# Optimization experiments

Measured on AMD Instinct MI355X. Metric: run time of the kernel, lower is better.

Reference implementation:

```python
import jax, jax.numpy as jnp
import numpy as np

B, M, H, R = 4096, 4, 1024, 10
MID, D3 = 512, 3 * H  # gate MLP mid = max(32, H//2)
AUDIO = 1
OTHERS = (0, 2, 3)


def _ln(x, w, b):
    m = jnp.mean(x, axis=-1, keepdims=True)
    v = jnp.mean((x - m) ** 2, axis=-1, keepdims=True)
    return (x - m) * jax.lax.rsqrt(v + 1e-5) * w + b


def _gate(t, s, lw, lb, w1, b1, w2, b2):
    feat = jnp.concatenate([t, s, jnp.abs(t - s)], axis=-1)  # [..., 3H]
    h = jax.nn.gelu(_ln(feat, lw, lb) @ w1.T + b1, approximate=False)
    return jax.nn.sigmoid(h @ w2.T + b2)  # [..., 1]


def setup_inputs() -> dict:
    key = jax.random.key(0)
    ks = jax.random.split(key, 16)
    xn = lambda k, shp, fan: jax.random.normal(k, shp, jnp.float32) * (1.0 / np.sqrt(fan))
    inp = {
        'tokens': jax.random.normal(ks[0], (B, M, H), jnp.float32),
        'token_mask': jax.random.randint(ks[1], (B, M), 0, 2) > 0,
        # gate_other: LayerNorm(3H) -> Linear(3H,MID) -> GELU -> Linear(MID,1)
        'ln_go_w': jnp.ones((D3,), jnp.float32), 'ln_go_b': jnp.zeros((D3,), jnp.float32),
        'go_w1': xn(ks[2], (MID, D3), D3), 'go_b1': jnp.zeros((MID,), jnp.float32),
        'go_w2': xn(ks[3], (1, MID), MID), 'go_b2': jnp.zeros((1,), jnp.float32),
        # gate_audio
        'ln_ga_w': jnp.ones((D3,), jnp.float32), 'ln_ga_b': jnp.zeros((D3,), jnp.float32),
        'ga_w1': xn(ks[4], (MID, D3), D3), 'ga_b1': jnp.zeros((MID,), jnp.float32),
        'ga_w2': xn(ks[5], (1, MID), MID), 'ga_b2': jnp.zeros((1,), jnp.float32),
        'a2o_w': xn(ks[6], (H, H), H), 'o2a_w': xn(ks[7], (H, H), H),
        'ln_o_w': jnp.ones((H,), jnp.float32), 'ln_o_b': jnp.zeros((H,), jnp.float32),
        'ln_a_w': jnp.ones((H,), jnp.float32), 'ln_a_b': jnp.zeros((H,), jnp.float32),
        # LMF
        'factors': jax.random.normal(ks[8], (M, R, H + 1, H), jnp.float32) * np.sqrt(2.0 / (H + 1 + H)),
        'rank_w': jax.random.normal(ks[9], (R,), jnp.float32) * 0.02,
        'lmf_bias': jnp.zeros((H,), jnp.float32),
        'out_ln1_w': jnp.ones((H,), jnp.float32), 'out_ln1_b': jnp.zeros((H,), jnp.float32),
        'out_w': xn(ks[10], (H, H), H), 'out_b': jnp.zeros((H,), jnp.float32),
        'out_ln2_w': jnp.ones((H,), jnp.float32), 'out_ln2_b': jnp.zeros((H,), jnp.float32),
    }
    return inp


def reference(tokens, token_mask, ln_go_w, ln_go_b, go_w1, go_b1, go_w2, go_b2,
              ln_ga_w, ln_ga_b, ga_w1, ga_b1, ga_w2, ga_b2, a2o_w, o2a_w,
              ln_o_w, ln_o_b, ln_a_w, ln_a_b, factors, rank_w, lmf_bias,
              out_ln1_w, out_ln1_b, out_w, out_b, out_ln2_w, out_ln2_b):
    mask_f = token_mask.astype(tokens.dtype)  # [B, M]
    oidx = jnp.asarray(OTHERS)

    # ---- AudioGuidedResidualMixer (eval mode) ----
    audio = tokens[:, AUDIO]                          # [B, H]
    audio_valid = token_mask[:, AUDIO]                # [B]
    others = tokens[:, oidx] * mask_f[:, oidx, None]  # [B, 3, H] (masked targets)
    src = jnp.broadcast_to(audio[:, None, :], others.shape)
    g = _gate(others, src, ln_go_w, ln_go_b, go_w1, go_b1, go_w2, go_b2)  # [B,3,1]
    a2o = audio @ a2o_w.T                                                  # [B, H]
    upd = _ln(others + g * a2o[:, None, :], ln_o_w, ln_o_b)
    pair_valid = token_mask[:, oidx] & audio_valid[:, None]                # [B, 3]
    others_new = jnp.where(pair_valid[..., None], upd, others) * mask_f[:, oidx, None]

    w_o = mask_f[:, oidx, None]
    denom = jnp.clip(w_o.sum(axis=1), 1.0, None)
    others_mean = (others_new * w_o).sum(axis=1) / denom                   # [B, H]
    aum = audio_valid & token_mask[:, oidx].any(axis=1)                    # [B]
    g_a = _gate(audio, others_mean, ln_ga_w, ln_ga_b, ga_w1, ga_b1, ga_w2, ga_b2)
    o2a = others_mean @ o2a_w.T
    mixed_audio = jnp.where(aum[:, None],
                            _ln(audio + g_a * o2a, ln_a_w, ln_a_b),
                            audio * mask_f[:, AUDIO, None])
    mixed = jnp.stack([others_new[:, 0], mixed_audio, others_new[:, 1], others_new[:, 2]],
                      axis=1) * mask_f[..., None]                          # [B, M, H]

    # ---- LowRankMultiplicativeFusion ----
    one = jnp.ones((mixed.shape[0], M, 1), mixed.dtype)
    x_aug = jnp.concatenate([one, mixed], axis=-1)                         # [B, M, H+1]
    z = jnp.einsum('bmd,mrdh->bmrh', x_aug, factors)                       # [B, M, R, H]
    z = jnp.where(token_mask[:, :, None, None], z, jnp.ones((), z.dtype))
    rank_tensor = jnp.prod(z, axis=1)                                      # [B, R, H]
    fused = jnp.einsum('brh,r->bh', rank_tensor, rank_w) + lmf_bias
    h = _ln(fused, out_ln1_w, out_ln1_b)
    h = jax.nn.gelu(h @ out_w.T + out_b, approximate=False)
    return _ln(h, out_ln2_w, out_ln2_b)                                    # [B, H]
```

## Files before the change

kernel.cpp:

```cpp
#include <hip/hip_runtime.h>
#include <math.h>

#define BB 4096
#define HH 1024
#define RR 10
#define MIDD 512
#define D3 3072

typedef __bf16 bf16x8 __attribute__((ext_vector_type(8)));
typedef __bf16 bf16x4 __attribute__((ext_vector_type(4)));
typedef float f32x4 __attribute__((ext_vector_type(4)));

__device__ __forceinline__ float waveSum(float v){
#pragma unroll
  for(int o=32;o>0;o>>=1) v += __shfl_down(v,o,64);
  return v;
}
__device__ __forceinline__ float blockSum256(float v, float* sc){
  v = waveSum(v);
  __syncthreads();
  if((threadIdx.x & 63)==0) sc[threadIdx.x>>6] = v;
  __syncthreads();
  return sc[0]+sc[1]+sc[2]+sc[3];
}
__device__ __forceinline__ float gelu_f(float x){
  return 0.5f*x*(1.0f+erff(x*0.70710678118654752f));
}
__device__ __forceinline__ void gl_lds16(const void* g, void* lds){
  __builtin_amdgcn_global_load_lds((const __attribute__((address_space(1))) unsigned int*)g,
                                   (__attribute__((address_space(3))) unsigned int*)lds,
                                   16, 0, 0);
}

__global__ void convw_k(const float* __restrict__ s0, __bf16* __restrict__ d0, int n0,
                        const float* __restrict__ s1, __bf16* __restrict__ d1, int n1,
                        const float* __restrict__ s2, __bf16* __restrict__ d2, int n2,
                        const float* __restrict__ s3, __bf16* __restrict__ d3, int n3,
                        const float* __restrict__ s4, __bf16* __restrict__ d4, int n4){
  long i = ((long)blockIdx.x*256 + threadIdx.x)*4;
  const float* s; __bf16* d;
  if(i<n0){ s=s0; d=d0; }
  else { i-=n0; if(i<n1){ s=s1; d=d1; }
  else { i-=n1; if(i<n2){ s=s2; d=d2; }
  else { i-=n2; if(i<n3){ s=s3; d=d3; }
  else { i-=n3; if(i>=n4) return; s=s4; d=d4; } } } }
  float4 v=*(const float4*)(s+i);
  bf16x4 o; o[0]=(__bf16)v.x; o[1]=(__bf16)v.y; o[2]=(__bf16)v.z; o[3]=(__bf16)v.w;
  *(bf16x4*)(d+i)=o;
}

__global__ void feat_go_k(const float* __restrict__ tokens, const int* __restrict__ mask,
                          const float* __restrict__ lnw, const float* __restrict__ lnb,
                          __bf16* __restrict__ featGo, __bf16* __restrict__ audioB,
                          float* __restrict__ gpre){
  int row=blockIdx.x; int b=row/3; int j=row-b*3; int oj=(j==0)?0:(j+1);
  if(threadIdx.x==0) gpre[row]=0.f;
  const float* to=tokens+((size_t)b*4+oj)*HH;
  const float* ta=tokens+((size_t)b*4+1)*HH;
  float mo = mask[b*4+oj]?1.f:0.f;
  int tid=threadIdx.x;
  __shared__ float sc[4];
  float ov[4], av[4], dv[4]; float s=0.f,s2=0.f;
#pragma unroll
  for(int p=0;p<4;p++){
    int h=tid+p*256;
    float o=to[h]*mo, a=ta[h], d=fabsf(o-a);
    ov[p]=o; av[p]=a; dv[p]=d;
    s+=o+a+d; s2+=o*o+a*a+d*d;
  }
  s=blockSum256(s,sc); s2=blockSum256(s2,sc);
  float mean=s/(float)D3, rstd=rsqrtf(s2/(float)D3-mean*mean+1e-5f);
  __bf16* fr = featGo + (size_t)row*D3;
#pragma unroll
  for(int p=0;p<4;p++){
    int h=tid+p*256;
    fr[h]       =(__bf16)((ov[p]-mean)*rstd*lnw[h]+lnb[h]);
    fr[1024+h]  =(__bf16)((av[p]-mean)*rstd*lnw[1024+h]+lnb[1024+h]);
    fr[2048+h]  =(__bf16)((dv[p]-mean)*rstd*lnw[2048+h]+lnb[2048+h]);
    if(j==0) audioB[(size_t)b*HH+h]=(__bf16)av[p];
  }
}

template<int ACT>
__launch_bounds__(256, 4)
__global__ void gemm_nt_mfma(const __bf16* __restrict__ A, int lda,
                             const __bf16* __restrict__ Bm, int ldb,
                             const float* __restrict__ bias,
                             float* __restrict__ C, int ldc, int K,
                             const float* __restrict__ w2,
                             float* __restrict__ gpre){
  __shared__ __align__(16) __bf16 As[3*2048];
  __shared__ __align__(16) __bf16 Bs[3*4096];
  const int tid=threadIdx.x, l=tid&63, w=tid>>6;
  const int wr=w>>1, wc=w&1;
  const int quad=l>>4, lr16=l&15;

  const int nbx = gridDim.x;
  const int flat = blockIdx.x + nbx*blockIdx.y;
  const int chunk = (nbx*gridDim.y)>>3;
  const int nid = (flat&7)*chunk + (flat>>3);
  const int bx = nid % nbx, by = nid / nbx;
  const int row0=by*64, col0=bx*128;

  const int srow=l>>2, sq=(l&3)^((l>>3)&3);
  const int nsteps = K>>5;

  const __bf16* pa  = A  + (size_t)(row0 + w*16       + srow)*lda + sq*8;
  const __bf16* pb0 = Bm + (size_t)(col0 + w*16       + srow)*ldb + sq*8;
  const __bf16* pb1 = Bm + (size_t)(col0 + (w+4)*16   + srow)*ldb + sq*8;
  __bf16* da  = As + ((size_t)w*64     + l)*8;
  __bf16* db0 = Bs + ((size_t)w*64     + l)*8;
  __bf16* db1 = Bs + ((size_t)(w+4)*64 + l)*8;

  auto stage=[&](int s,int bi){
    int k0 = s*32;
    gl_lds16(pa  + k0, da  + bi*2048);
    gl_lds16(pb0 + k0, db0 + bi*4096);
    gl_lds16(pb1 + k0, db1 + bi*4096);
  };

  f32x4 acc[2][4];
  f32x4 zerov={0.f,0.f,0.f,0.f};
#pragma unroll
  for(int i=0;i<2;i++)
#pragma unroll
    for(int j=0;j<4;j++) acc[i][j]=zerov;

  stage(0,0);
  stage(1,1);
  asm volatile("s_waitcnt vmcnt(3)" ::: "memory");
  __builtin_amdgcn_s_barrier();

  int cur=0;
  for(int step=0; step<nsteps; ++step){
    const __bf16* Ab = As + cur*2048;
    const __bf16* Bb = Bs + cur*4096;
    bf16x8 af[2], bg[4];
#pragma unroll
    for(int fi=0;fi<2;fi++){
      int R = wr*32 + fi*16 + lr16;
      af[fi]=*(const bf16x8*)(Ab + R*32 + ((quad^(R>>1))&3)*8);
    }
#pragma unroll
    for(int fj=0;fj<4;fj++){
      int N = wc*64 + fj*16 + lr16;
      bg[fj]=*(const bf16x8*)(Bb + N*32 + ((quad^(N>>1))&3)*8);
    }
    if(step+2<nsteps){
      int bi = cur + 2; if(bi>=3) bi-=3;
      stage(step+2, bi);
    }
    __builtin_amdgcn_s_setprio(1);
#pragma unroll
    for(int fi=0;fi<2;fi++)
#pragma unroll
      for(int fj=0;fj<4;fj++)
        acc[fi][fj]=__builtin_amdgcn_mfma_f32_16x16x32_bf16(af[fi],bg[fj],acc[fi][fj],0,0,0);
    __builtin_amdgcn_s_setprio(0);
    asm volatile("s_waitcnt lgkmcnt(0)" ::: "memory");
    if(step < nsteps-2) asm volatile("s_waitcnt vmcnt(3)" ::: "memory");
    else                asm volatile("s_waitcnt vmcnt(0)" ::: "memory");
    __builtin_amdgcn_s_barrier();
    cur = (cur+1==3)?0:cur+1;
  }

  if(ACT==2){
    float b1v[4], w2v[4];
#pragma unroll
    for(int fj=0;fj<4;fj++){
      int col=col0+wc*64+fj*16+lr16;
      b1v[fj]=bias[col]; w2v[fj]=w2[col];
    }
#pragma unroll
    for(int fi=0;fi<2;fi++){
#pragma unroll
      for(int reg=0;reg<4;reg++){
        float part=0.f;
#pragma unroll
        for(int fj=0;fj<4;fj++) part += gelu_f(acc[fi][fj][reg]+b1v[fj])*w2v[fj];
        part += __shfl_xor(part,1,64);
        part += __shfl_xor(part,2,64);
        part += __shfl_xor(part,4,64);
        part += __shfl_xor(part,8,64);
        if((l&15)==0) atomicAdd(&gpre[row0+wr*32+fi*16+quad*4+reg], part);
      }
    }
    return;
  }

  float bv[4];
#pragma unroll
  for(int fj=0;fj<4;fj++) bv[fj] = (ACT==1)? bias[col0+wc*64+fj*16+lr16] : 0.f;
#pragma unroll
  for(int fi=0;fi<2;fi++){
#pragma unroll
    for(int reg=0;reg<4;reg++){
      int row=row0+wr*32+fi*16+quad*4+reg;
#pragma unroll
      for(int fj=0;fj<4;fj++){
        int col=col0+wc*64+fj*16+lr16;
        float v=acc[fi][fj][reg];
        if(ACT==1) v=gelu_f(v+bv[fj]);
        C[(size_t)row*ldc+col]=v;
      }
    }
  }
}

__global__ void others_k(const float* __restrict__ tokens, const int* __restrict__ mask,
                         const float* __restrict__ gpre, const float* __restrict__ go_b2,
                         const float* __restrict__ a2o,
                         const float* __restrict__ lnw, const float* __restrict__ lnb,
                         const float* __restrict__ galnw, const float* __restrict__ galnb,
                         __bf16* __restrict__ mixedB, __bf16* __restrict__ omeanB,
                         __bf16* __restrict__ featGa, float* __restrict__ gapre){
  int b=blockIdx.x, tid=threadIdx.x;
  __shared__ float sc[4];
  if(tid==0) gapre[b]=0.f;
  float ma = mask[b*4+1]?1.f:0.f;
  float a2[4];
#pragma unroll
  for(int p=0;p<4;p++) a2[p]=a2o[(size_t)b*HH+tid+p*256];
  float sum[4]={0,0,0,0}; float cnt=0.f;
  for(int j=0;j<3;j++){
    int oj=(j==0)?0:(j+1);
    float mo=mask[b*4+oj]?1.f:0.f; cnt+=mo;
    float gv=1.f/(1.f+expf(-(gpre[b*3+j]+go_b2[0])));
    float t[4], ov[4]; float s=0.f,s2=0.f;
#pragma unroll
    for(int p=0;p<4;p++){
      int h=tid+p*256;
      float o=tokens[((size_t)b*4+oj)*HH+h]*mo;
      ov[p]=o; t[p]=o+gv*a2[p];
      s+=t[p]; s2+=t[p]*t[p];
    }
    s=blockSum256(s,sc); s2=blockSum256(s2,sc);
    float mean=s/1024.f, rstd=rsqrtf(s2/1024.f-mean*mean+1e-5f);
    float pv=mo*ma;
#pragma unroll
    for(int p=0;p<4;p++){
      int h=tid+p*256;
      float upd=(t[p]-mean)*rstd*lnw[h]+lnb[h];
      float on=((pv>0.5f)?upd:ov[p])*mo;
      mixedB[(size_t)b*4096 + (size_t)oj*HH + h]=(__bf16)on;
      sum[p]+=on*mo;
    }
  }
  float denom=fmaxf(cnt,1.f);
  float vm[4];
#pragma unroll
  for(int p=0;p<4;p++){
    vm[p]=sum[p]/denom;
    omeanB[(size_t)b*HH+tid+p*256]=(__bf16)vm[p];
  }
  const float* ta=tokens+((size_t)b*4+1)*HH;
  float tv[4], dv[4]; float s=0.f,s2=0.f;
#pragma unroll
  for(int p=0;p<4;p++){
    int h=tid+p*256;
    float a=ta[h], d=fabsf(a-vm[p]);
    tv[p]=a; dv[p]=d;
    s+=a+vm[p]+d; s2+=a*a+vm[p]*vm[p]+d*d;
  }
  s=blockSum256(s,sc); s2=blockSum256(s2,sc);
  float mean=s/(float)D3, rstd=rsqrtf(s2/(float)D3-mean*mean+1e-5f);
  __bf16* fr=featGa+(size_t)b*D3;
#pragma unroll
  for(int p=0;p<4;p++){
    int h=tid+p*256;
    fr[h]     =(__bf16)((tv[p]-mean)*rstd*galnw[h]+galnb[h]);
    fr[1024+h]=(__bf16)((vm[p]-mean)*rstd*galnw[1024+h]+galnb[1024+h]);
    fr[2048+h]=(__bf16)((dv[p]-mean)*rstd*galnw[2048+h]+galnb[2048+h]);
  }
}

__global__ void audio_k(const float* __restrict__ tokens, const int* __restrict__ mask,
                        const float* __restrict__ gapre, const float* __restrict__ ga_b2,
                        const float* __restrict__ o2a,
                        const float* __restrict__ lnw, const float* __restrict__ lnb,
                        __bf16* __restrict__ mixedB,
                        const float* __restrict__ lmf_bias, float* __restrict__ fused){
  int b=blockIdx.x, tid=threadIdx.x;
  __shared__ float sc[4];
  int ma_i=mask[b*4+1];
  int any = mask[b*4+0]|mask[b*4+2]|mask[b*4+3];
  bool aum = (ma_i!=0) && (any!=0);
  float ma = ma_i?1.f:0.f;
  float gv=1.f/(1.f+expf(-(gapre[b]+ga_b2[0])));
  const float* ta = tokens + ((size_t)b*4+1)*HH;
  float av[4], t[4]; float s=0.f,s2=0.f;
#pragma unroll
  for(int p=0;p<4;p++){
    int h=tid+p*256;
    av[p]=ta[h];
    t[p]=av[p]+gv*o2a[(size_t)b*HH+h];
    s+=t[p]; s2+=t[p]*t[p];
  }
  s=blockSum256(s,sc); s2=blockSum256(s2,sc);
  float mean=s/1024.f, rstd=rsqrtf(s2/1024.f-mean*mean+1e-5f);
#pragma unroll
  for(int p=0;p<4;p++){
    int h=tid+p*256;
    float u=(t[p]-mean)*rstd*lnw[h]+lnb[h];
    float outv = aum ? u : av[p]*ma;
    mixedB[(size_t)b*4096 + HH + h]=(__bf16)(outv*ma);
    fused[(size_t)b*HH + h]=lmf_bias[h];
  }
}

__global__ void transpose_factors_k(const float* __restrict__ factors,
                                    __bf16* __restrict__ factT){
  __shared__ float T[64][65];
  int mr = blockIdx.z;
  int d0 = blockIdx.y*64, h0 = blockIdx.x*64;
  int t = threadIdx.x;
  int rr = t>>4, cc = (t&15)*4;
  const float* src = factors + ((size_t)mr*1025 + 1 + d0)*1024 + h0;
#pragma unroll
  for(int q=0;q<4;q++){
    float4 v = *(const float4*)(src + (size_t)(q*16+rr)*1024 + cc);
    T[q*16+rr][cc]=v.x; T[q*16+rr][cc+1]=v.y; T[q*16+rr][cc+2]=v.z; T[q*16+rr][cc+3]=v.w;
  }
  __syncthreads();
  __bf16* dst = factT + ((size_t)mr*1024 + h0)*1024 + d0;
#pragma unroll
  for(int q=0;q<4;q++){
    int hr = q*16 + rr;
    bf16x4 o;
    o[0]=(__bf16)T[cc][hr];   o[1]=(__bf16)T[cc+1][hr];
    o[2]=(__bf16)T[cc+2][hr]; o[3]=(__bf16)T[cc+3][hr];
    *(bf16x4*)(dst + (size_t)hr*1024 + cc) = o;
  }
}

__launch_bounds__(256, 2)
__global__ void gemm_lmf2(const __bf16* __restrict__ mixedB,
                          const __bf16* __restrict__ factT,
                          const float* __restrict__ factors,
                          const int* __restrict__ mask,
                          const float* __restrict__ rank_w,
                          float* __restrict__ fused){
  __shared__ __align__(16) __bf16 As[3*4096];
  __shared__ __align__(16) __bf16 Bs[3*4096];
  __shared__ float Mskf[4][128];
  __shared__ float F0s[20][128];
  __shared__ float Rws[5];
  const int tid = threadIdx.x;
  const int l = tid & 63, w = tid >> 6;
  const int wr = w >> 1, wc = w & 1;
  const int quad = l >> 4, lr16 = l & 15;

  const int flat = blockIdx.x + 8*(blockIdx.y + 32*blockIdx.z);
  const int nid  = (flat & 7)*64 + (flat >> 3);
  const int hh   = nid >> 6;
  const int rest = nid & 63;
  const int by   = rest >> 1;
  const int bz   = rest & 1;
  const int row0 = by * 128, col0 = hh * 128;
  const int z5   = bz * 5;

  const int srow = l >> 2;
  const int sq   = (l & 3) ^ ((l >> 3) & 3);

  for(int i = tid; i < 512; i += 256){
    int mm = i >> 7, rl = i & 127;
    Mskf[mm][rl] = mask[(row0 + rl)*4 + mm] ? 1.f : 0.f;
  }
  for(int i = tid; i < 2560; i += 256){
    int rm = i >> 7, cl = i & 127;
    int m = rm & 3, rg = z5 + (rm >> 2);
    F0s[rm][cl] = factors[(size_t)(m*RR + rg)*1025*1024 + col0 + cl];
  }
  if(tid < 5) Rws[tid] = rank_w[z5 + tid];

  const __bf16* pa0 = mixedB + (size_t)(row0 + w*16     + srow)*4096 + sq*8;
  const __bf16* pa1 = mixedB + (size_t)(row0 + (w+4)*16 + srow)*4096 + sq*8;
  const __bf16* pb0 = factT + ((size_t)(col0 + w*16     + srow))*1024 + sq*8;
  const __bf16* pb1 = factT + ((size_t)(col0 + (w+4)*16 + srow))*1024 + sq*8;
  __bf16* da0 = As + ((size_t)w*64     + l)*8;
  __bf16* da1 = As + ((size_t)(w+4)*64 + l)*8;
  __bf16* db0 = Bs + ((size_t)w*64     + l)*8;
  __bf16* db1 = Bs + ((size_t)(w+4)*64 + l)*8;

  auto stage = [&](int s, int bi){
    int rm = s >> 5, k0 = (s & 31)*32;
    int m = rm & 3, rg = z5 + (rm >> 2);
    size_t ao = (size_t)m*1024 + k0;
    size_t bo = (size_t)(m*RR + rg)*1048576 + k0;
    gl_lds16(pa0 + ao, da0 + bi*4096);
    gl_lds16(pa1 + ao, da1 + bi*4096);
    gl_lds16(pb0 + bo, db0 + bi*4096);
    gl_lds16(pb1 + bo, db1 + bi*4096);
  };

  f32x4 fsum[4][4];
  f32x4 prod[4][4];
  f32x4 acc[4][4];
  f32x4 zerov = {0.f,0.f,0.f,0.f};
#pragma unroll
  for(int i=0;i<4;i++)
#pragma unroll
    for(int j=0;j<4;j++) fsum[i][j] = zerov;

  stage(0, 0);
  stage(1, 1);
  asm volatile("s_waitcnt vmcnt(4)" ::: "memory");
  asm volatile("s_waitcnt lgkmcnt(0)" ::: "memory");
  __builtin_amdgcn_s_barrier();

  int cur = 0;
  for(int step = 0; step < 640; ++step){
    const __bf16* Ab = As + cur*4096;
    const __bf16* Bb = Bs + cur*4096;
    bf16x8 af[4], bg[4];
#pragma unroll
    for(int fi=0;fi<4;fi++){
      int R = wr*64 + fi*16 + lr16;
      af[fi] = *(const bf16x8*)(Ab + R*32 + ((quad ^ (R>>1)) & 3)*8);
    }
#pragma unroll
    for(int fj=0;fj<4;fj++){
      int N = wc*64 + fj*16 + lr16;
      bg[fj] = *(const bf16x8*)(Bb + N*32 + ((quad ^ (N>>1)) & 3)*8);
    }
    if(step + 2 < 640){
      int bi = cur + 2; if(bi >= 3) bi -= 3;
      stage(step + 2, bi);
    }
    if((step & 127) == 0){
      f32x4 onev = {1.f,1.f,1.f,1.f};
#pragma unroll
      for(int fi=0;fi<4;fi++)
#pragma unroll
        for(int fj=0;fj<4;fj++) prod[fi][fj] = onev;
    }
    if((step & 31) == 0){
      int rm = step >> 5;
#pragma unroll
      for(int fj=0;fj<4;fj++){
        float f0 = F0s[rm][wc*64 + fj*16 + lr16];
        f32x4 iv = {f0,f0,f0,f0};
#pragma unroll
        for(int fi=0;fi<4;fi++) acc[fi][fj] = iv;
      }
    }
    __builtin_amdgcn_s_setprio(1);
#pragma unroll
    for(int fi=0;fi<4;fi++)
#pragma unroll
      for(int fj=0;fj<4;fj++)
        acc[fi][fj] = __builtin_amdgcn_mfma_f32_16x16x32_bf16(af[fi], bg[fj], acc[fi][fj], 0,0,0);
    __builtin_amdgcn_s_setprio(0);
    if((step & 31) == 31){
      int mm = (step >> 5) & 3;
#pragma unroll
      for(int fi=0;fi<4;fi++)
#pragma unroll
        for(int reg=0;reg<4;reg++){
          float mk = Mskf[mm][wr*64 + fi*16 + quad*4 + reg];
#pragma unroll
          for(int fj=0;fj<4;fj++)
            prod[fi][fj][reg] *= (mk != 0.f) ? acc[fi][fj][reg] : 1.f;
        }
    }
    if((step & 127) == 127){
      float rw = Rws[step >> 7];
#pragma unroll
      for(int fi=0;fi<4;fi++)
#pragma unroll
        for(int fj=0;fj<4;fj++)
#pragma unroll
          for(int reg=0;reg<4;reg++)
            fsum[fi][fj][reg] += rw * prod[fi][fj][reg];
    }
    asm volatile("s_waitcnt lgkmcnt(0)" ::: "memory");
    if(step < 638) asm volatile("s_waitcnt vmcnt(4)" ::: "memory");
    else           asm volatile("s_waitcnt vmcnt(0)" ::: "memory");
    __builtin_amdgcn_s_barrier();
    cur = (cur + 1 == 3) ? 0 : cur + 1;
  }

#pragma unroll
  for(int fi=0;fi<4;fi++){
#pragma unroll
    for(int reg=0;reg<4;reg++){
      int row = row0 + wr*64 + fi*16 + quad*4 + reg;
#pragma unroll
      for(int fj=0;fj<4;fj++){
        int col = col0 + wc*64 + fj*16 + lr16;
        atomicAdd(&fused[(size_t)row*HH + col], fsum[fi][fj][reg]);
      }
    }
  }
}

__global__ void ln_row_k(const float* __restrict__ X, const float* __restrict__ w,
                         const float* __restrict__ bb, float* __restrict__ Y){
  int b=blockIdx.x, tid=threadIdx.x;
  __shared__ float sc[4];
  const float* x=X+(size_t)b*HH;
  float t[4]; float s=0.f,s2=0.f;
#pragma unroll
  for(int p=0;p<4;p++){ t[p]=x[tid+p*256]; s+=t[p]; s2+=t[p]*t[p]; }
  s=blockSum256(s,sc); s2=blockSum256(s2,sc);
  float mean=s/1024.f, rstd=rsqrtf(s2/1024.f-mean*mean+1e-5f);
#pragma unroll
  for(int p=0;p<4;p++){
    int h=tid+p*256;
    Y[(size_t)b*HH+h]=(t[p]-mean)*rstd*w[h]+bb[h];
  }
}
__global__ void ln_row_bf16_k(const float* __restrict__ X, const float* __restrict__ w,
                              const float* __restrict__ bb, __bf16* __restrict__ Y){
  int b=blockIdx.x, tid=threadIdx.x;
  __shared__ float sc[4];
  const float* x=X+(size_t)b*HH;
  float t[4]; float s=0.f,s2=0.f;
#pragma unroll
  for(int p=0;p<4;p++){ t[p]=x[tid+p*256]; s+=t[p]; s2+=t[p]*t[p]; }
  s=blockSum256(s,sc); s2=blockSum256(s2,sc);
  float mean=s/1024.f, rstd=rsqrtf(s2/1024.f-mean*mean+1e-5f);
#pragma unroll
  for(int p=0;p<4;p++){
    int h=tid+p*256;
    Y[(size_t)b*HH+h]=(__bf16)((t[p]-mean)*rstd*w[h]+bb[h]);
  }
}

extern "C" void kernel_launch(void* const* d_in, const int* in_sizes, int n_in,
                              void* d_out, int out_size, void* d_ws, size_t ws_size,
                              hipStream_t stream) {
  const float* tokens   =(const float*)d_in[0];
  const int*   mask     =(const int*)  d_in[1];
  const float* ln_go_w  =(const float*)d_in[2];
  const float* ln_go_b  =(const float*)d_in[3];
  const float* go_w1    =(const float*)d_in[4];
  const float* go_b1    =(const float*)d_in[5];
  const float* go_w2    =(const float*)d_in[6];
  const float* go_b2    =(const float*)d_in[7];
  const float* ln_ga_w  =(const float*)d_in[8];
  const float* ln_ga_b  =(const float*)d_in[9];
  const float* ga_w1    =(const float*)d_in[10];
  const float* ga_b1    =(const float*)d_in[11];
  const float* ga_w2    =(const float*)d_in[12];
  const float* ga_b2    =(const float*)d_in[13];
  const float* a2o_w    =(const float*)d_in[14];
  const float* o2a_w    =(const float*)d_in[15];
  const float* ln_o_w   =(const float*)d_in[16];
  const float* ln_o_b   =(const float*)d_in[17];
  const float* ln_a_w   =(const float*)d_in[18];
  const float* ln_a_b   =(const float*)d_in[19];
  const float* factors  =(const float*)d_in[20];
  const float* rank_w   =(const float*)d_in[21];
  const float* lmf_bias =(const float*)d_in[22];
  const float* out_ln1_w=(const float*)d_in[23];
  const float* out_ln1_b=(const float*)d_in[24];
  const float* out_w    =(const float*)d_in[25];
  const float* out_b    =(const float*)d_in[26];
  const float* out_ln2_w=(const float*)d_in[27];
  const float* out_ln2_b=(const float*)d_in[28];
  float* out=(float*)d_out;

  char* wsp=(char*)d_ws; size_t off=0;
  auto alloc=[&](size_t bytes)->void*{
    void* p=wsp+off; off=(off+bytes+255)&~(size_t)255; return p;
  };
  __bf16* factT   =(__bf16*)alloc((size_t)4*RR*HH*HH*2);
  __bf16* featGo  =(__bf16*)alloc((size_t)BB*3*D3*2);
  __bf16* featGa  =(__bf16*)alloc((size_t)BB*D3*2);
  float*  g_go_pre=(float*) alloc((size_t)BB*3*4);
  float*  ga_pre  =(float*) alloc((size_t)BB*4);
  float*  a2o     =(float*) alloc((size_t)BB*HH*4);
  __bf16* mixedB  =(__bf16*)alloc((size_t)BB*4*HH*2);
  __bf16* omeanB  =(__bf16*)alloc((size_t)BB*HH*2);
  __bf16* audioB  =(__bf16*)alloc((size_t)BB*HH*2);
  float*  o2a     =(float*) alloc((size_t)BB*HH*4);
  float*  fused   =(float*) alloc((size_t)BB*HH*4);
  __bf16* hbufB   =(__bf16*)alloc((size_t)BB*HH*2);
  __bf16* go_w1B  =(__bf16*)alloc((size_t)MIDD*D3*2);
  __bf16* ga_w1B  =(__bf16*)alloc((size_t)MIDD*D3*2);
  __bf16* a2o_wB  =(__bf16*)alloc((size_t)HH*HH*2);
  __bf16* o2a_wB  =(__bf16*)alloc((size_t)HH*HH*2);
  __bf16* out_wB  =(__bf16*)alloc((size_t)HH*HH*2);

  {
    int n0=MIDD*D3, n1=MIDD*D3, n2=HH*HH, n3=HH*HH, n4=HH*HH;
    int total4=(n0+n1+n2+n3+n4)/4;
    convw_k<<<(total4+255)/256,256,0,stream>>>(go_w1,go_w1B,n0, ga_w1,ga_w1B,n1,
                                               a2o_w,a2o_wB,n2, o2a_w,o2a_wB,n3,
                                               out_w,out_wB,n4);
  }
  transpose_factors_k<<<dim3(16,16,40),256,0,stream>>>(factors,factT);
  feat_go_k<<<BB*3,256,0,stream>>>(tokens,mask,ln_go_w,ln_go_b,featGo,audioB,g_go_pre);
  gemm_nt_mfma<0><<<dim3(8,64),256,0,stream>>>(audioB,HH,a2o_wB,HH,nullptr,a2o,HH,HH,nullptr,nullptr);
  gemm_nt_mfma<2><<<dim3(4,192),256,0,stream>>>(featGo,D3,go_w1B,D3,go_b1,nullptr,0,D3,go_w2,g_go_pre);
  others_k<<<BB,256,0,stream>>>(tokens,mask,g_go_pre,go_b2,a2o,ln_o_w,ln_o_b,
                                ln_ga_w,ln_ga_b,mixedB,omeanB,featGa,ga_pre);
  gemm_nt_mfma<2><<<dim3(4,64),256,0,stream>>>(featGa,D3,ga_w1B,D3,ga_b1,nullptr,0,D3,ga_w2,ga_pre);
  gemm_nt_mfma<0><<<dim3(8,64),256,0,stream>>>(omeanB,HH,o2a_wB,HH,nullptr,o2a,HH,HH,nullptr,nullptr);
  audio_k<<<BB,256,0,stream>>>(tokens,mask,ga_pre,ga_b2,o2a,ln_a_w,ln_a_b,mixedB,lmf_bias,fused);
  gemm_lmf2<<<dim3(8,32,2),256,0,stream>>>(mixedB,factT,factors,mask,rank_w,fused);
  ln_row_bf16_k<<<BB,256,0,stream>>>(fused,out_ln1_w,out_ln1_b,hbufB);
  gemm_nt_mfma<1><<<dim3(8,64),256,0,stream>>>(hbufB,HH,out_wB,HH,out_b,fused,HH,HH,nullptr,nullptr);
  ln_row_k<<<BB,256,0,stream>>>(fused,out_ln2_w,out_ln2_b,out);
}
```

Baseline: 1.021 ms.

## Merge prep kernels and pair independent GEMMs into combined launches

Weight conversion, factor transposition and gate-feature LayerNorm are folded into one prep kernel selected by block index. Independent GEMM pairs (a2o with gate_other hidden, gate_audio hidden with o2a) run in one launch through a runtime descriptor, so they fill the GPU together and pay fewer launch gaps. The LMF GEMM block-to-tile mapping is also reordered for locality. The GEMM activation mode becomes a runtime branch instead of a template parameter, which may cost registers or code quality.

```diff
diff --git a/kernel.cpp b/kernel.cpp
--- a/kernel.cpp
+++ b/kernel.cpp
@@ -32,82 +32,118 @@
                                    16, 0, 0);
 }
 
-__global__ void convw_k(const float* __restrict__ s0, __bf16* __restrict__ d0, int n0,
-                        const float* __restrict__ s1, __bf16* __restrict__ d1, int n1,
-                        const float* __restrict__ s2, __bf16* __restrict__ d2, int n2,
-                        const float* __restrict__ s3, __bf16* __restrict__ d3, int n3,
-                        const float* __restrict__ s4, __bf16* __restrict__ d4, int n4){
-  long i = ((long)blockIdx.x*256 + threadIdx.x)*4;
-  const float* s; __bf16* d;
-  if(i<n0){ s=s0; d=d0; }
-  else { i-=n0; if(i<n1){ s=s1; d=d1; }
-  else { i-=n1; if(i<n2){ s=s2; d=d2; }
-  else { i-=n2; if(i<n3){ s=s3; d=d3; }
-  else { i-=n3; if(i>=n4) return; s=s4; d=d4; } } } }
-  float4 v=*(const float4*)(s+i);
-  bf16x4 o; o[0]=(__bf16)v.x; o[1]=(__bf16)v.y; o[2]=(__bf16)v.z; o[3]=(__bf16)v.w;
-  *(bf16x4*)(d+i)=o;
-}
-
-__global__ void feat_go_k(const float* __restrict__ tokens, const int* __restrict__ mask,
-                          const float* __restrict__ lnw, const float* __restrict__ lnb,
-                          __bf16* __restrict__ featGo, __bf16* __restrict__ audioB,
-                          float* __restrict__ gpre){
-  int row=blockIdx.x; int b=row/3; int j=row-b*3; int oj=(j==0)?0:(j+1);
-  if(threadIdx.x==0) gpre[row]=0.f;
-  const float* to=tokens+((size_t)b*4+oj)*HH;
-  const float* ta=tokens+((size_t)b*4+1)*HH;
-  float mo = mask[b*4+oj]?1.f:0.f;
-  int tid=threadIdx.x;
-  __shared__ float sc[4];
-  float ov[4], av[4], dv[4]; float s=0.f,s2=0.f;
-#pragma unroll
-  for(int p=0;p<4;p++){
-    int h=tid+p*256;
-    float o=to[h]*mo, a=ta[h], d=fabsf(o-a);
-    ov[p]=o; av[p]=a; dv[p]=d;
-    s+=o+a+d; s2+=o*o+a*a+d*d;
-  }
-  s=blockSum256(s,sc); s2=blockSum256(s2,sc);
-  float mean=s/(float)D3, rstd=rsqrtf(s2/(float)D3-mean*mean+1e-5f);
-  __bf16* fr = featGo + (size_t)row*D3;
-#pragma unroll
-  for(int p=0;p<4;p++){
-    int h=tid+p*256;
-    fr[h]       =(__bf16)((ov[p]-mean)*rstd*lnw[h]+lnb[h]);
-    fr[1024+h]  =(__bf16)((av[p]-mean)*rstd*lnw[1024+h]+lnb[1024+h]);
-    fr[2048+h]  =(__bf16)((dv[p]-mean)*rstd*lnw[2048+h]+lnb[2048+h]);
-    if(j==0) audioB[(size_t)b*HH+h]=(__bf16)av[p];
-  }
-}
-
-template<int ACT>
+__global__ void prep_k(const float* __restrict__ go_w1, __bf16* __restrict__ go_w1B,
+                       const float* __restrict__ ga_w1, __bf16* __restrict__ ga_w1B,
+                       const float* __restrict__ a2o_w, __bf16* __restrict__ a2o_wB,
+                       const float* __restrict__ o2a_w, __bf16* __restrict__ o2a_wB,
+                       const float* __restrict__ out_w, __bf16* __restrict__ out_wB,
+                       const float* __restrict__ factors, __bf16* __restrict__ factT,
+                       const float* __restrict__ tokens, const int* __restrict__ mask,
+                       const float* __restrict__ lnw, const float* __restrict__ lnb,
+                       __bf16* __restrict__ featGo, __bf16* __restrict__ audioB,
+                       float* __restrict__ gpre){
+  __shared__ float T[64][65];
+  const int b = blockIdx.x;
+  const int tid = threadIdx.x;
+
+  if(b < 6144){
+    const int n0=MIDD*D3, n1=MIDD*D3, n2=HH*HH, n3=HH*HH, n4=HH*HH;
+    long i = ((long)b*256 + tid)*4;
+    const float* s; __bf16* d;
+    if(i<n0){ s=go_w1; d=go_w1B; }
+    else { i-=n0; if(i<n1){ s=ga_w1; d=ga_w1B; }
+    else { i-=n1; if(i<n2){ s=a2o_w; d=a2o_wB; }
+    else { i-=n2; if(i<n3){ s=o2a_w; d=o2a_wB; }
+    else { i-=n3; if(i>=n4) return; s=out_w; d=out_wB; } } } }
+    float4 v=*(const float4*)(s+i);
+    bf16x4 o; o[0]=(__bf16)v.x; o[1]=(__bf16)v.y; o[2]=(__bf16)v.z; o[3]=(__bf16)v.w;
+    *(bf16x4*)(d+i)=o;
+    return;
+  }
+  if(b < 16384){
+    int id = b - 6144;
+    int h0 = (id & 15)*64;
+    int d0 = ((id >> 4) & 15)*64;
+    int mr = id >> 8;
+    int rr = tid>>4, cc = (tid&15)*4;
+    const float* src = factors + ((size_t)mr*1025 + 1 + d0)*1024 + h0;
+#pragma unroll
+    for(int q=0;q<4;q++){
+      float4 v = *(const float4*)(src + (size_t)(q*16+rr)*1024 + cc);
+      T[q*16+rr][cc]=v.x; T[q*16+rr][cc+1]=v.y; T[q*16+rr][cc+2]=v.z; T[q*16+rr][cc+3]=v.w;
+    }
+    __syncthreads();
+    __bf16* dst = factT + ((size_t)mr*1024 + h0)*1024 + d0;
+#pragma unroll
+    for(int q=0;q<4;q++){
+      int hr = q*16 + rr;
+      bf16x4 o;
+      o[0]=(__bf16)T[cc][hr];   o[1]=(__bf16)T[cc+1][hr];
+      o[2]=(__bf16)T[cc+2][hr]; o[3]=(__bf16)T[cc+3][hr];
+      *(bf16x4*)(dst + (size_t)hr*1024 + cc) = o;
+    }
+    return;
+  }
+  {
+    int row = b - 16384;
+    int bb_ = row/3; int j = row - bb_*3; int oj = (j==0)?0:(j+1);
+    if(tid==0) gpre[row]=0.f;
+    const float* to=tokens+((size_t)bb_*4+oj)*HH;
+    const float* ta=tokens+((size_t)bb_*4+1)*HH;
+    float mo = mask[bb_*4+oj]?1.f:0.f;
+    float* sc = &T[0][0];
+    float ov[4], av[4], dv[4]; float s=0.f,s2=0.f;
+#pragma unroll
+    for(int p=0;p<4;p++){
+      int h=tid+p*256;
+      float o=to[h]*mo, a=ta[h], d=fabsf(o-a);
+      ov[p]=o; av[p]=a; dv[p]=d;
+      s+=o+a+d; s2+=o*o+a*a+d*d;
+    }
+    s=blockSum256(s,sc); s2=blockSum256(s2,sc);
+    float mean=s/(float)D3, rstd=rsqrtf(s2/(float)D3-mean*mean+1e-5f);
+    __bf16* fr = featGo + (size_t)row*D3;
+#pragma unroll
+    for(int p=0;p<4;p++){
+      int h=tid+p*256;
+      fr[h]       =(__bf16)((ov[p]-mean)*rstd*lnw[h]+lnb[h]);
+      fr[1024+h]  =(__bf16)((av[p]-mean)*rstd*lnw[1024+h]+lnb[1024+h]);
+      fr[2048+h]  =(__bf16)((dv[p]-mean)*rstd*lnw[2048+h]+lnb[2048+h]);
+      if(j==0) audioB[(size_t)bb_*HH+h]=(__bf16)av[p];
+    }
+  }
+}
+
+struct GD {
+  const __bf16* A; const __bf16* B;
+  const float* bias; float* C;
+  const float* w2; float* gpre;
+  int lda, ldb, ldc, K, nbx, nby, act;
+};
+
 __launch_bounds__(256, 4)
-__global__ void gemm_nt_mfma(const __bf16* __restrict__ A, int lda,
-                             const __bf16* __restrict__ Bm, int ldb,
-                             const float* __restrict__ bias,
-                             float* __restrict__ C, int ldc, int K,
-                             const float* __restrict__ w2,
-                             float* __restrict__ gpre){
+__global__ void gemm_dual_k(GD d0, GD d1, int n0){
   __shared__ __align__(16) __bf16 As[3*2048];
   __shared__ __align__(16) __bf16 Bs[3*4096];
   const int tid=threadIdx.x, l=tid&63, w=tid>>6;
   const int wr=w>>1, wc=w&1;
   const int quad=l>>4, lr16=l&15;
 
-  const int nbx = gridDim.x;
-  const int flat = blockIdx.x + nbx*blockIdx.y;
-  const int chunk = (nbx*gridDim.y)>>3;
-  const int nid = (flat&7)*chunk + (flat>>3);
-  const int bx = nid % nbx, by = nid / nbx;
+  GD d; int lb;
+  if((int)blockIdx.x < n0){ d = d0; lb = blockIdx.x; }
+  else                    { d = d1; lb = blockIdx.x - n0; }
+
+  const int chunk = (d.nbx*d.nby)>>3;
+  const int nid = (lb&7)*chunk + (lb>>3);
+  const int bx = nid % d.nbx, by = nid / d.nbx;
   const int row0=by*64, col0=bx*128;
 
   const int srow=l>>2, sq=(l&3)^((l>>3)&3);
-  const int nsteps = K>>5;
-
-  const __bf16* pa  = A  + (size_t)(row0 + w*16       + srow)*lda + sq*8;
-  const __bf16* pb0 = Bm + (size_t)(col0 + w*16       + srow)*ldb + sq*8;
-  const __bf16* pb1 = Bm + (size_t)(col0 + (w+4)*16   + srow)*ldb + sq*8;
+  const int nsteps = d.K>>5;
+
+  const __bf16* pa  = d.A + (size_t)(row0 + w*16       + srow)*d.lda + sq*8;
+  const __bf16* pb0 = d.B + (size_t)(col0 + w*16       + srow)*d.ldb + sq*8;
+  const __bf16* pb1 = d.B + (size_t)(col0 + (w+4)*16   + srow)*d.ldb + sq*8;
   __bf16* da  = As + ((size_t)w*64     + l)*8;
   __bf16* db0 = Bs + ((size_t)w*64     + l)*8;
   __bf16* db1 = Bs + ((size_t)(w+4)*64 + l)*8;
@@ -164,12 +200,12 @@
     cur = (cur+1==3)?0:cur+1;
   }
 
-  if(ACT==2){
+  if(d.act==2){
     float b1v[4], w2v[4];
 #pragma unroll
     for(int fj=0;fj<4;fj++){
       int col=col0+wc*64+fj*16+lr16;
-      b1v[fj]=bias[col]; w2v[fj]=w2[col];
+      b1v[fj]=d.bias[col]; w2v[fj]=d.w2[col];
     }
 #pragma unroll
     for(int fi=0;fi<2;fi++){
@@ -182,7 +218,7 @@
         part += __shfl_xor(part,2,64);
         part += __shfl_xor(part,4,64);
         part += __shfl_xor(part,8,64);
-        if((l&15)==0) atomicAdd(&gpre[row0+wr*32+fi*16+quad*4+reg], part);
+        if((l&15)==0) atomicAdd(&d.gpre[row0+wr*32+fi*16+quad*4+reg], part);
       }
     }
     return;
@@ -190,7 +226,7 @@
 
   float bv[4];
 #pragma unroll
-  for(int fj=0;fj<4;fj++) bv[fj] = (ACT==1)? bias[col0+wc*64+fj*16+lr16] : 0.f;
+  for(int fj=0;fj<4;fj++) bv[fj] = (d.act==1)? d.bias[col0+wc*64+fj*16+lr16] : 0.f;
 #pragma unroll
   for(int fi=0;fi<2;fi++){
 #pragma unroll
@@ -200,8 +236,8 @@
       for(int fj=0;fj<4;fj++){
         int col=col0+wc*64+fj*16+lr16;
         float v=acc[fi][fj][reg];
-        if(ACT==1) v=gelu_f(v+bv[fj]);
-        C[(size_t)row*ldc+col]=v;
+        if(d.act==1) v=gelu_f(v+bv[fj]);
+        d.C[(size_t)row*d.ldc+col]=v;
       }
     }
   }
@@ -305,31 +341,6 @@
     float outv = aum ? u : av[p]*ma;
     mixedB[(size_t)b*4096 + HH + h]=(__bf16)(outv*ma);
     fused[(size_t)b*HH + h]=lmf_bias[h];
-  }
-}
-
-__global__ void transpose_factors_k(const float* __restrict__ factors,
-                                    __bf16* __restrict__ factT){
-  __shared__ float T[64][65];
-  int mr = blockIdx.z;
-  int d0 = blockIdx.y*64, h0 = blockIdx.x*64;
-  int t = threadIdx.x;
-  int rr = t>>4, cc = (t&15)*4;
-  const float* src = factors + ((size_t)mr*1025 + 1 + d0)*1024 + h0;
-#pragma unroll
-  for(int q=0;q<4;q++){
-    float4 v = *(const float4*)(src + (size_t)(q*16+rr)*1024 + cc);
-    T[q*16+rr][cc]=v.x; T[q*16+rr][cc+1]=v.y; T[q*16+rr][cc+2]=v.z; T[q*16+rr][cc+3]=v.w;
-  }
-  __syncthreads();
-  __bf16* dst = factT + ((size_t)mr*1024 + h0)*1024 + d0;
-#pragma unroll
-  for(int q=0;q<4;q++){
-    int hr = q*16 + rr;
-    bf16x4 o;
-    o[0]=(__bf16)T[cc][hr];   o[1]=(__bf16)T[cc+1][hr];
-    o[2]=(__bf16)T[cc+2][hr]; o[3]=(__bf16)T[cc+3][hr];
-    *(bf16x4*)(dst + (size_t)hr*1024 + cc) = o;
   }
 }
 
@@ -351,11 +362,11 @@
   const int quad = l >> 4, lr16 = l & 15;
 
   const int flat = blockIdx.x + 8*(blockIdx.y + 32*blockIdx.z);
-  const int nid  = (flat & 7)*64 + (flat >> 3);
-  const int hh   = nid >> 6;
-  const int rest = nid & 63;
-  const int by   = rest >> 1;
-  const int bz   = rest & 1;
+  const int x    = flat & 7;
+  const int j    = flat >> 3;
+  const int bz   = x & 1;
+  const int by   = (x >> 1)*8 + (j >> 3);
+  const int hh   = j & 7;
   const int row0 = by * 128, col0 = hh * 128;
   const int z5   = bz * 5;
 
@@ -400,7 +411,7 @@
 #pragma unroll
   for(int i=0;i<4;i++)
 #pragma unroll
-    for(int j=0;j<4;j++) fsum[i][j] = zerov;
+    for(int j2=0;j2<4;j2++) fsum[i][j2] = zerov;
 
   stage(0, 0);
   stage(1, 1);
@@ -583,24 +594,33 @@
   __bf16* o2a_wB  =(__bf16*)alloc((size_t)HH*HH*2);
   __bf16* out_wB  =(__bf16*)alloc((size_t)HH*HH*2);
 
+  prep_k<<<28672,256,0,stream>>>(go_w1,go_w1B, ga_w1,ga_w1B, a2o_w,a2o_wB,
+                                 o2a_w,o2a_wB, out_w,out_wB,
+                                 factors,factT,
+                                 tokens,mask,ln_go_w,ln_go_b,featGo,audioB,g_go_pre);
   {
-    int n0=MIDD*D3, n1=MIDD*D3, n2=HH*HH, n3=HH*HH, n4=HH*HH;
-    int total4=(n0+n1+n2+n3+n4)/4;
-    convw_k<<<(total4+255)/256,256,0,stream>>>(go_w1,go_w1B,n0, ga_w1,ga_w1B,n1,
-                                               a2o_w,a2o_wB,n2, o2a_w,o2a_wB,n3,
-                                               out_w,out_wB,n4);
-  }
-  transpose_factors_k<<<dim3(16,16,40),256,0,stream>>>(factors,factT);
-  feat_go_k<<<BB*3,256,0,stream>>>(tokens,mask,ln_go_w,ln_go_b,featGo,audioB,g_go_pre);
-  gemm_nt_mfma<0><<<dim3(8,64),256,0,stream>>>(audioB,HH,a2o_wB,HH,nullptr,a2o,HH,HH,nullptr,nullptr);
-  gemm_nt_mfma<2><<<dim3(4,192),256,0,stream>>>(featGo,D3,go_w1B,D3,go_b1,nullptr,0,D3,go_w2,g_go_pre);
+    GD dA = { audioB, a2o_wB, nullptr, a2o, nullptr, nullptr,
+              HH, HH, HH, HH, 8, 64, 0 };
+    GD dH = { featGo, go_w1B, go_b1, nullptr, go_w2, g_go_pre,
+              D3, D3, 0, D3, 4, 192, 2 };
+    gemm_dual_k<<<512+768,256,0,stream>>>(dA, dH, 512);
+  }
   others_k<<<BB,256,0,stream>>>(tokens,mask,g_go_pre,go_b2,a2o,ln_o_w,ln_o_b,
                                 ln_ga_w,ln_ga_b,mixedB,omeanB,featGa,ga_pre);
-  gemm_nt_mfma<2><<<dim3(4,64),256,0,stream>>>(featGa,D3,ga_w1B,D3,ga_b1,nullptr,0,D3,ga_w2,ga_pre);
-  gemm_nt_mfma<0><<<dim3(8,64),256,0,stream>>>(omeanB,HH,o2a_wB,HH,nullptr,o2a,HH,HH,nullptr,nullptr);
+  {
+    GD dH = { featGa, ga_w1B, ga_b1, nullptr, ga_w2, ga_pre,
+              D3, D3, 0, D3, 4, 64, 2 };
+    GD dO = { omeanB, o2a_wB, nullptr, o2a, nullptr, nullptr,
+              HH, HH, HH, HH, 8, 64, 0 };
+    gemm_dual_k<<<256+512,256,0,stream>>>(dH, dO, 256);
+  }
   audio_k<<<BB,256,0,stream>>>(tokens,mask,ga_pre,ga_b2,o2a,ln_a_w,ln_a_b,mixedB,lmf_bias,fused);
   gemm_lmf2<<<dim3(8,32,2),256,0,stream>>>(mixedB,factT,factors,mask,rank_w,fused);
   ln_row_bf16_k<<<BB,256,0,stream>>>(fused,out_ln1_w,out_ln1_b,hbufB);
-  gemm_nt_mfma<1><<<dim3(8,64),256,0,stream>>>(hbufB,HH,out_wB,HH,out_b,fused,HH,HH,nullptr,nullptr);
+  {
+    GD dO = { hbufB, out_wB, out_b, fused, nullptr, nullptr,
+              HH, HH, HH, HH, 8, 64, 1 };
+    gemm_dual_k<<<512,256,0,stream>>>(dO, dO, 512);
+  }
   ln_row_k<<<BB,256,0,stream>>>(fused,out_ln2_w,out_ln2_b,out);
 }
```

Result: no change. 1.010 ms (-1.1%).
